# Performance work log

Hardware: AMD Instinct MI355X
Metric: run time of the kernel (lower is better)

Reference implementation:

```python
import jax, jax.numpy as jnp
import numpy as np

B, N, DIM, H, DH = 16, 1024, 768, 12, 64
SCALE = DH ** -0.5


def setup_inputs() -> dict:
    key = jax.random.key(0)
    k1, k2, k3 = jax.random.split(key, 3)
    x = jax.random.normal(k1, (B, N, DIM), dtype=jnp.float32)
    W_qkv = jax.random.normal(k2, (DIM, 3 * H * DH), dtype=jnp.float32) * (DIM ** -0.5)
    W_out = jax.random.normal(k3, (H * DH, DIM), dtype=jnp.float32) * ((H * DH) ** -0.5)
    b_out = jnp.zeros((DIM,), dtype=jnp.float32)
    # perm = [0] + random shuffle of 1..N-1 (matches module's construction)
    rng = np.random.default_rng(0)
    perm = jnp.asarray(np.concatenate([[0], rng.permutation(np.arange(1, N))]), dtype=jnp.int32)
    return {"x": x, "W_qkv": W_qkv, "W_out": W_out, "b_out": b_out, "perm": perm}


def reference(x, W_qkv, W_out, b_out, perm):
    # QKV projection: [b, n, 3*h*d]
    qkv = jnp.einsum('bnd,de->bne', x, W_qkv)
    q, k, v = jnp.split(qkv, 3, axis=-1)
    # [b, n, h*d] -> [b, h, n, d]
    reshape = lambda t: t.reshape(B, N, H, DH).transpose(0, 2, 1, 3)
    q, k, v = reshape(q), reshape(k), reshape(v)
    # permute query rows
    q = q[:, :, perm]
    dots = jnp.einsum('bhqd,bhkd->bhqk', q, k) * SCALE
    attn = jax.nn.softmax(dots, axis=-1)
    out = jnp.einsum('bhqk,bhkd->bhqd', attn, v)
    out = out.transpose(0, 2, 1, 3).reshape(B, N, H * DH)
    return jnp.einsum('bne,ed->bnd', out, W_out) + b_out
```

## Files before the change

### kernel.cpp

```cpp
#include <hip/hip_runtime.h>
#include <hip/hip_bf16.h>


typedef __bf16 bf16x8 __attribute__((ext_vector_type(8)));
typedef __bf16 bf16x4 __attribute__((ext_vector_type(4)));
typedef float  f32x4  __attribute__((ext_vector_type(4)));

__device__ __forceinline__ f32x4 mfma16(bf16x8 a, bf16x8 b, f32x4 c) {
    return __builtin_amdgcn_mfma_f32_16x16x32_bf16(a, b, c, 0, 0, 0);
}

__device__ __forceinline__ void async16(const void* g, void* l) {
    __builtin_amdgcn_global_load_lds(
        (const __attribute__((address_space(1))) unsigned int*)g,
        (__attribute__((address_space(3))) unsigned int*)l,
        16, 0, 0);
}

__global__ __launch_bounds__(256)
void prep(const void* __restrict__ x, __bf16* __restrict__ Xc,
          const void* __restrict__ Wqkv, __bf16* __restrict__ Wqt,
          const void* __restrict__ Wout, __bf16* __restrict__ Wot,
          int* __restrict__ flag) {
    __shared__ __bf16 tile[64][65];
    __shared__ int cnt;
    const int bid = blockIdx.x;
    const int tid = threadIdx.x;

    const unsigned short* raw =
        (bid < 1024) ? (const unsigned short*)x
                     : (bid < 1456) ? (const unsigned short*)Wqkv
                                    : (const unsigned short*)Wout;
    if (tid == 0) cnt = 0;
    __syncthreads();
    int local = 0;
    for (int i = tid; i < 2048; i += 256) {
        unsigned e = (raw[i] >> 7) & 0xFFu;
        if (e >= 0xC0u) local++;
    }
    atomicAdd(&cnt, local);
    __syncthreads();
    const int f = (cnt > 16) ? 1 : 0;
    if (bid == 0 && tid == 0) *flag = f;

    if (bid < 1024) {
        const int n4 = 16384 * 768 / 4;
        int i = bid * 256 + tid;
        const int stride = 1024 * 256;
        if (f) {
            const float4* s = (const float4*)x;
            for (; i < n4; i += stride) {
                float4 v = s[i];
                bf16x4 o;
                o[0] = (__bf16)v.x; o[1] = (__bf16)v.y;
                o[2] = (__bf16)v.z; o[3] = (__bf16)v.w;
                *(bf16x4*)&Xc[(size_t)i * 4] = o;
            }
        } else {
            const ushort4* s = (const ushort4*)x;
            for (; i < n4; i += stride) *(ushort4*)&Xc[(size_t)i * 4] = s[i];
        }
    } else {
        const void* in;
        __bf16* out;
        int R, C, c0, r0;
        if (bid < 1456) {
            int t = bid - 1024;
            in = Wqkv; out = Wqt; R = 768; C = 2304;
            c0 = (t % 36) * 64; r0 = (t / 36) * 64;
        } else {
            int t = bid - 1456;
            in = Wout; out = Wot; R = 768; C = 768;
            c0 = (t % 12) * 64; r0 = (t / 12) * 64;
        }
        const int tx = tid & 63, ty = tid >> 6;
#pragma unroll
        for (int k = 0; k < 16; ++k) {
            int r = ty + 4 * k;
            size_t idx = (size_t)(r0 + r) * C + c0 + tx;
            tile[r][tx] = f ? (__bf16)((const float*)in)[idx] : ((const __bf16*)in)[idx];
        }
        __syncthreads();
#pragma unroll
        for (int k = 0; k < 16; ++k) {
            int cc = ty + 4 * k;
            out[(size_t)(c0 + cc) * R + r0 + tx] = tile[tx][cc];
        }
    }
}

#define GMFMA16()                                                       \
    acc[0][0] = mfma16(af0, bf0, acc[0][0]);                            \
    acc[0][1] = mfma16(af0, bf1, acc[0][1]);                            \
    acc[0][2] = mfma16(af0, bf2, acc[0][2]);                            \
    acc[0][3] = mfma16(af0, bf3, acc[0][3]);                            \
    acc[1][0] = mfma16(af1, bf0, acc[1][0]);                            \
    acc[1][1] = mfma16(af1, bf1, acc[1][1]);                            \
    acc[1][2] = mfma16(af1, bf2, acc[1][2]);                            \
    acc[1][3] = mfma16(af1, bf3, acc[1][3]);                            \
    acc[2][0] = mfma16(af2, bf0, acc[2][0]);                            \
    acc[2][1] = mfma16(af2, bf1, acc[2][1]);                            \
    acc[2][2] = mfma16(af2, bf2, acc[2][2]);                            \
    acc[2][3] = mfma16(af2, bf3, acc[2][3]);                            \
    acc[3][0] = mfma16(af3, bf0, acc[3][0]);                            \
    acc[3][1] = mfma16(af3, bf1, acc[3][1]);                            \
    acc[3][2] = mfma16(af3, bf2, acc[3][2]);                            \
    acc[3][3] = mfma16(af3, bf3, acc[3][3])

#define GTILE(RD, ST, DO_STAGE, VMK) do {                               \
    if ((VMK) == 4)                                                     \
        asm volatile("s_waitcnt vmcnt(4) lgkmcnt(0)" ::: "memory");     \
    else                                                                \
        asm volatile("s_waitcnt vmcnt(0) lgkmcnt(0)" ::: "memory");     \
    __builtin_amdgcn_s_barrier();                                       \
    if (DO_STAGE) {                                                     \
        async16(gA0, smem + (ST) + stA0);                               \
        async16(gA1, smem + (ST) + stA1);                               \
        async16(gB0, smem + (ST) + 8192 + stA0);                        \
        async16(gB1, smem + (ST) + 8192 + stA1);                        \
        gA0 += 32; gA1 += 32; gB0 += 32; gB1 += 32;                     \
    }                                                                   \
    bf16x8 af0 = *(const bf16x8*)(smem + (RD) + aoff0);                 \
    bf16x8 af1 = *(const bf16x8*)(smem + (RD) + aoff1);                 \
    bf16x8 af2 = *(const bf16x8*)(smem + (RD) + aoff2);                 \
    bf16x8 af3 = *(const bf16x8*)(smem + (RD) + aoff3);                 \
    bf16x8 bf0 = *(const bf16x8*)(smem + (RD) + boff0);                 \
    bf16x8 bf1 = *(const bf16x8*)(smem + (RD) + boff1);                 \
    bf16x8 bf2 = *(const bf16x8*)(smem + (RD) + boff2);                 \
    bf16x8 bf3 = *(const bf16x8*)(smem + (RD) + boff3);                 \
    GMFMA16();                                                          \
} while (0)

template <int MODE>
__global__ __launch_bounds__(256, 3)
void gemm_bt(const __bf16* __restrict__ A, int lda,
             const __bf16* __restrict__ Bt,
             const void* __restrict__ bias,
             void* __restrict__ Cout, int ldc,
             int K, const int* __restrict__ flag,
             __bf16* __restrict__ vt) {
    __shared__ __align__(16) char smem[49152];
    const int tid  = threadIdx.x;
    const int wid  = tid >> 6;
    const int lane = tid & 63;
    const int quad = lane >> 4;
    const int l15  = lane & 15;

    const int bm = blockIdx.x * 128;
    const int bn = blockIdx.y * 128;

    const int wm = (wid & 1) * 64;
    const int wn = (wid >> 1) * 64;
    const int srow  = lane >> 2;
    const int sslot = lane & 3;

    const int rA0 = wid * 16 + srow;
    const int rA1 = 64 + wid * 16 + srow;
    const __bf16* gA0 = A  + (size_t)(bm + rA0) * lda + ((sslot ^ ((rA0 >> 1) & 3)) << 3);
    const __bf16* gA1 = A  + (size_t)(bm + rA1) * lda + ((sslot ^ ((rA1 >> 1) & 3)) << 3);
    const __bf16* gB0 = Bt + (size_t)(bn + rA0) * K   + ((sslot ^ ((rA0 >> 1) & 3)) << 3);
    const __bf16* gB1 = Bt + (size_t)(bn + rA1) * K   + ((sslot ^ ((rA1 >> 1) & 3)) << 3);
    const int stA0 = (wid * 16) * 64;
    const int stA1 = (64 + wid * 16) * 64;

    const int rf0 = wm + 0 * 16 + l15, rf1 = wm + 1 * 16 + l15;
    const int rf2 = wm + 2 * 16 + l15, rf3 = wm + 3 * 16 + l15;
    const int aoff0 = rf0 * 64 + ((quad ^ ((rf0 >> 1) & 3)) * 16);
    const int aoff1 = rf1 * 64 + ((quad ^ ((rf1 >> 1) & 3)) * 16);
    const int aoff2 = rf2 * 64 + ((quad ^ ((rf2 >> 1) & 3)) * 16);
    const int aoff3 = rf3 * 64 + ((quad ^ ((rf3 >> 1) & 3)) * 16);
    const int rg0 = wn + 0 * 16 + l15, rg1 = wn + 1 * 16 + l15;
    const int rg2 = wn + 2 * 16 + l15, rg3 = wn + 3 * 16 + l15;
    const int boff0 = 8192 + rg0 * 64 + ((quad ^ ((rg0 >> 1) & 3)) * 16);
    const int boff1 = 8192 + rg1 * 64 + ((quad ^ ((rg1 >> 1) & 3)) * 16);
    const int boff2 = 8192 + rg2 * 64 + ((quad ^ ((rg2 >> 1) & 3)) * 16);
    const int boff3 = 8192 + rg3 * 64 + ((quad ^ ((rg3 >> 1) & 3)) * 16);

    f32x4 acc[4][4];
#pragma unroll
    for (int i = 0; i < 4; ++i)
#pragma unroll
        for (int j = 0; j < 4; ++j) acc[i][j] = (f32x4)0.0f;

    async16(gA0, smem + stA0);
    async16(gA1, smem + stA1);
    async16(gB0, smem + 8192 + stA0);
    async16(gB1, smem + 8192 + stA1);
    gA0 += 32; gA1 += 32; gB0 += 32; gB1 += 32;
    async16(gA0, smem + 16384 + stA0);
    async16(gA1, smem + 16384 + stA1);
    async16(gB0, smem + 16384 + 8192 + stA0);
    async16(gB1, smem + 16384 + 8192 + stA1);
    gA0 += 32; gA1 += 32; gB0 += 32; gB1 += 32;

#pragma unroll 1
    for (int g = 0; g < 7; ++g) {
        GTILE(0,     32768, true, 4);
        GTILE(16384, 0,     true, 4);
        GTILE(32768, 16384, true, 4);
    }
    GTILE(0,     32768, true,  4);
    GTILE(16384, 0,     false, 4);
    GTILE(32768, 0,     false, 0);

    if (MODE == 0 && bn >= 1536) {
        const int bq = bm >> 10;
        const int n0 = (bm & 1023) + wm + quad * 4;
        const int colb = bn - 1536 + wn;
#pragma unroll
        for (int mi = 0; mi < 4; ++mi)
#pragma unroll
            for (int ni = 0; ni < 4; ++ni) {
                int col = colb + ni * 16 + l15;
                bf16x4 v;
                v[0] = (__bf16)acc[mi][ni][0];
                v[1] = (__bf16)acc[mi][ni][1];
                v[2] = (__bf16)acc[mi][ni][2];
                v[3] = (__bf16)acc[mi][ni][3];
                *(bf16x4*)&vt[((size_t)bq * 768 + col) * 1024 + n0 + mi * 16] = v;
            }
        return;
    }

    const int f = (MODE == 1) ? *flag : 0;
    if (MODE == 1) {
#pragma unroll
        for (int ni = 0; ni < 4; ++ni) {
            int col = bn + wn + ni * 16 + l15;
            float bv = f ? ((const float*)bias)[col] : (float)((const __bf16*)bias)[col];
#pragma unroll
            for (int mi = 0; mi < 4; ++mi)
#pragma unroll
                for (int rg = 0; rg < 4; ++rg) acc[mi][ni][rg] += bv;
        }
    }

    if (MODE == 0 || !f) {
        __bf16* cs = (__bf16*)smem;
#pragma unroll
        for (int c = 0; c < 4; ++c) {
            __syncthreads();
            if (wm == (c >> 1) * 64) {
                int mb = (c & 1) * 2;
#pragma unroll
                for (int mloc = 0; mloc < 2; ++mloc) {
                    int rowc = mloc * 16 + quad * 4;
#pragma unroll
                    for (int ni = 0; ni < 4; ++ni) {
                        int col = wn + ni * 16 + l15;
#pragma unroll
                        for (int rg = 0; rg < 4; ++rg)
                            cs[(rowc + rg) * 136 + col] = (__bf16)acc[mb + mloc][ni][rg];
                    }
                }
            }
            __syncthreads();
#pragma unroll
            for (int p = 0; p < 2; ++p) {
                int row  = p * 16 + (tid >> 4);
                int colc = tid & 15;
                bf16x8 v = *(const bf16x8*)&cs[row * 136 + colc * 8];
                *(bf16x8*)((__bf16*)Cout + (size_t)(bm + c * 32 + row) * ldc + bn + colc * 8) = v;
            }
        }
    } else {
        float* cs = (float*)smem;
#pragma unroll
        for (int c = 0; c < 8; ++c) {
            __syncthreads();
            if (wm == (c >> 2) * 64) {
                int mi = c & 3;
                int rowc = quad * 4;
#pragma unroll
                for (int ni = 0; ni < 4; ++ni) {
                    int col = wn + ni * 16 + l15;
#pragma unroll
                    for (int rg = 0; rg < 4; ++rg)
                        cs[(rowc + rg) * 132 + col] = acc[mi][ni][rg];
                }
            }
            __syncthreads();
#pragma unroll
            for (int p = 0; p < 2; ++p) {
                int row  = p * 8 + (tid >> 5);
                int colc = tid & 31;
                float4 v = *(const float4*)&cs[row * 132 + colc * 4];
                *(float4*)((float*)Cout + (size_t)(bm + c * 16 + row) * ldc + bn + colc * 4) = v;
            }
        }
    }
}

__global__ __launch_bounds__(256, 2)
void attn(const __bf16* qkv, const __bf16* __restrict__ vt,
          const int* __restrict__ perm, __bf16* O, int ldo) {
    __shared__ __align__(16) char smem[55296];
    __bf16* Qs = (__bf16*)smem;
    __bf16* Ps = (__bf16*)(smem + 32768);

    const int tid  = threadIdx.x;
    const int wid  = tid >> 6;
    const int lane = tid & 63;
    const int quad = lane >> 4;
    const int l15  = lane & 15;
    const int bh = blockIdx.x;
    const int q0 = blockIdx.y * 128;
    const int b = bh / 12, h = bh % 12;
    const size_t row_base = (size_t)b * 1024;
    const int qcol = h * 64;
    const int kcol = 768 + h * 64;
    const int srow8  = lane >> 3;
    const int sslot8 = lane & 7;
    __bf16* Pw = Ps + wid * (32 * 88);

#pragma unroll
    for (int is = 0; is < 4; ++is) {
        int r = is * 32 + wid * 8 + srow8;
        int gr = perm[q0 + r];
        int chunk = sslot8 ^ (r & 7);
        async16(qkv + (row_base + gr) * 2304 + qcol + chunk * 8,
                &Qs[(is * 32 + wid * 8) * 64]);
    }
    __syncthreads();

    bf16x8 qf[2][2];
#pragma unroll
    for (int mi = 0; mi < 2; ++mi) {
        int r = wid * 32 + mi * 16 + l15;
#pragma unroll
        for (int ks = 0; ks < 2; ++ks)
            qf[mi][ks] = *(const bf16x8*)&Qs[r * 64 + (((ks * 4 + quad) ^ (r & 7)) * 8)];
    }
    asm volatile("s_waitcnt lgkmcnt(0)" ::: "memory");
    __builtin_amdgcn_sched_barrier(0);
    __builtin_amdgcn_s_barrier();

    const int off0 = l15 * 64 + (((0 * 4 + quad) ^ (l15 & 7)) * 8);
    const int off1 = l15 * 64 + (((1 * 4 + quad) ^ (l15 & 7)) * 8);
    const int pwb  = l15 * 88 + quad * 4;
    const int pfb  = l15 * 88 + quad * 8;

    const int rK = wid * 8 + srow8;
    const int ck = sslot8 ^ (rK & 7);
    const __bf16* kg0 = qkv + (row_base + rK) * 2304 + kcol + ck * 8;
    const __bf16* kg1 = kg0 + (size_t)32 * 2304;
    const __bf16* vg0 = vt + ((size_t)bh * 64 + rK) * 1024 + ck * 8;
    const __bf16* vg1 = vg0 + (size_t)32 * 1024;

    f32x4 acco[2][4];
#pragma unroll
    for (int mi = 0; mi < 2; ++mi)
#pragma unroll
        for (int ni = 0; ni < 4; ++ni) acco[mi][ni] = (f32x4)0.0f;
    float lsum[2] = {0.0f, 0.0f};

    const float cfac = 0.125f * 1.44269504088896340736f;

#define ASTAGE(KB, VB) do {                                             \
        async16(kg0, smem + (KB) + wid * 1024);                         \
        async16(kg1, smem + (KB) + 4096 + wid * 1024);                  \
        async16(vg0, smem + (VB) + wid * 1024);                         \
        async16(vg1, smem + (VB) + 4096 + wid * 1024);                  \
        kg0 += (size_t)64 * 2304; kg1 += (size_t)64 * 2304;             \
        vg0 += 64; vg1 += 64;                                           \
    } while (0)

    auto compute = [&](const __bf16* Kb, const __bf16* Vb) {
#pragma unroll
        for (int half = 0; half < 2; ++half) {
            f32x4 accs[2][2];
#pragma unroll
            for (int ki = 0; ki < 2; ++ki)
#pragma unroll
                for (int mi = 0; mi < 2; ++mi) accs[ki][mi] = (f32x4)0.0f;
#pragma unroll
            for (int ks = 0; ks < 2; ++ks) {
                const int off = ks ? off1 : off0;
                bf16x8 kf0 = *(const bf16x8*)&Kb[(half * 2 + 0) * 1024 + off];
                bf16x8 kf1 = *(const bf16x8*)&Kb[(half * 2 + 1) * 1024 + off];
                accs[0][0] = mfma16(kf0, qf[0][ks], accs[0][0]);
                accs[0][1] = mfma16(kf0, qf[1][ks], accs[0][1]);
                accs[1][0] = mfma16(kf1, qf[0][ks], accs[1][0]);
                accs[1][1] = mfma16(kf1, qf[1][ks], accs[1][1]);
            }

#pragma unroll
            for (int ki = 0; ki < 2; ++ki)
#pragma unroll
                for (int mi = 0; mi < 2; ++mi) {
                    bf16x4 pk;
                    float s0 = __builtin_amdgcn_exp2f(accs[ki][mi][0] * cfac - 8.0f);
                    float s1 = __builtin_amdgcn_exp2f(accs[ki][mi][1] * cfac - 8.0f);
                    float s2 = __builtin_amdgcn_exp2f(accs[ki][mi][2] * cfac - 8.0f);
                    float s3 = __builtin_amdgcn_exp2f(accs[ki][mi][3] * cfac - 8.0f);
                    pk[0] = (__bf16)s0; pk[1] = (__bf16)s1;
                    pk[2] = (__bf16)s2; pk[3] = (__bf16)s3;
                    lsum[mi] += (s0 + s1) + (s2 + s3);
                    *(bf16x4*)&Pw[pwb + mi * 1408 + (half * 2 + ki) * 16] = pk;
                }

            {
                bf16x8 pf0 = *(const bf16x8*)&Pw[pfb + 0 * 1408 + half * 32];
                bf16x8 pf1 = *(const bf16x8*)&Pw[pfb + 1 * 1408 + half * 32];
                const int offv = half ? off1 : off0;
#pragma unroll
                for (int ni = 0; ni < 4; ++ni) {
                    bf16x8 vf = *(const bf16x8*)&Vb[ni * 1024 + offv];
                    acco[0][ni] = mfma16(pf0, vf, acco[0][ni]);
                    acco[1][ni] = mfma16(pf1, vf, acco[1][ni]);
                }
            }
        }
    };

    ASTAGE(0, 16384);

#pragma unroll 1
    for (int kt2 = 0; kt2 < 8; ++kt2) {
        asm volatile("s_waitcnt vmcnt(0) lgkmcnt(0)" ::: "memory");
        __builtin_amdgcn_s_barrier();
        ASTAGE(8192, 16384 + 8192);
        compute((const __bf16*)smem, (const __bf16*)(smem + 16384));
        asm volatile("s_waitcnt vmcnt(0) lgkmcnt(0)" ::: "memory");
        __builtin_amdgcn_s_barrier();
        if (kt2 < 7) ASTAGE(0, 16384);
        compute((const __bf16*)(smem + 8192), (const __bf16*)(smem + 16384 + 8192));
    }
#undef ASTAGE

#pragma unroll
    for (int off = 16; off < 64; off <<= 1) {
        lsum[0] += __shfl_xor(lsum[0], off, 64);
        lsum[1] += __shfl_xor(lsum[1], off, 64);
    }

#pragma unroll
    for (int mi = 0; mi < 2; ++mi) {
#pragma unroll
        for (int rg = 0; rg < 4; ++rg) {
            float inv = 1.0f / __shfl(lsum[mi], quad * 4 + rg, 64);
            int orow = q0 + wid * 32 + mi * 16 + quad * 4 + rg;
#pragma unroll
            for (int ni = 0; ni < 4; ++ni) {
                int ocol = h * 64 + ni * 16 + l15;
                O[(row_base + orow) * (size_t)ldo + ocol] = (__bf16)(acco[mi][ni][rg] * inv);
            }
        }
    }
}

extern "C" void kernel_launch(void* const* d_in, const int* in_sizes, int n_in,
                              void* d_out, int out_size, void* d_ws, size_t ws_size,
                              hipStream_t stream) {
    (void)in_sizes; (void)n_in; (void)out_size; (void)ws_size;
    const void* x_raw    = d_in[0];
    const void* Wqkv_raw = d_in[1];
    const void* Wout_raw = d_in[2];
    const void* bout_raw = d_in[3];
    const int*  perm     = (const int*)d_in[4];

    char* ws = (char*)d_ws;
    int*    flag = (int*)ws;
    __bf16* Xc   = (__bf16*)(ws + 256);
    __bf16* QKV  = (__bf16*)(ws + 25166080);
    __bf16* Vt   = (__bf16*)(ws + 100663552);
    __bf16* Wqt  = (__bf16*)(ws + 125829376);
    __bf16* Wot  = (__bf16*)(ws + 129368320);
    __bf16* Obuf = QKV + 1536;

    prep<<<1600, 256, 0, stream>>>(x_raw, Xc, Wqkv_raw, Wqt, Wout_raw, Wot, flag);
    gemm_bt<0><<<dim3(128, 18), 256, 0, stream>>>(Xc, 768, Wqt, nullptr, QKV, 2304, 768, nullptr, Vt);
    attn<<<dim3(192, 8), 256, 0, stream>>>(QKV, Vt, perm, Obuf, 2304);
    gemm_bt<1><<<dim3(128, 6), 256, 0, stream>>>(Obuf, 2304, Wot, bout_raw, d_out, 768, 768, flag, nullptr);
}
```

Before: 198.0 us.

## Enlarge GEMM block tile to 256x128 with 128x64 per-warp tiles

Both projection GEMMs now use 256-row block tiles, so each warp computes a 128x64 sub-tile with 8x4 MFMA accumulators, and the grids are halved to match. The goal is more MFMA work per LDS fragment load and per staged byte, cutting LDS and global traffic per FLOP. The cost is a larger LDS footprint (72KB triple buffer), more registers, occupancy lowered from 3 to 2 blocks per CU, and fewer blocks in the grid (1152 and 384), which may leave CUs idle in the tail.

```diff
diff --git a/kernel.cpp b/kernel.cpp
--- a/kernel.cpp
+++ b/kernel.cpp
@@ -89,126 +89,108 @@
     }
 }
 
-#define GMFMA16()                                                       \
-    acc[0][0] = mfma16(af0, bf0, acc[0][0]);                            \
-    acc[0][1] = mfma16(af0, bf1, acc[0][1]);                            \
-    acc[0][2] = mfma16(af0, bf2, acc[0][2]);                            \
-    acc[0][3] = mfma16(af0, bf3, acc[0][3]);                            \
-    acc[1][0] = mfma16(af1, bf0, acc[1][0]);                            \
-    acc[1][1] = mfma16(af1, bf1, acc[1][1]);                            \
-    acc[1][2] = mfma16(af1, bf2, acc[1][2]);                            \
-    acc[1][3] = mfma16(af1, bf3, acc[1][3]);                            \
-    acc[2][0] = mfma16(af2, bf0, acc[2][0]);                            \
-    acc[2][1] = mfma16(af2, bf1, acc[2][1]);                            \
-    acc[2][2] = mfma16(af2, bf2, acc[2][2]);                            \
-    acc[2][3] = mfma16(af2, bf3, acc[2][3]);                            \
-    acc[3][0] = mfma16(af3, bf0, acc[3][0]);                            \
-    acc[3][1] = mfma16(af3, bf1, acc[3][1]);                            \
-    acc[3][2] = mfma16(af3, bf2, acc[3][2]);                            \
-    acc[3][3] = mfma16(af3, bf3, acc[3][3])
+#define GM4(MI, AF)                                                     \
+    acc[MI][0] = mfma16(AF, bq0, acc[MI][0]);                           \
+    acc[MI][1] = mfma16(AF, bq1, acc[MI][1]);                           \
+    acc[MI][2] = mfma16(AF, bq2, acc[MI][2]);                           \
+    acc[MI][3] = mfma16(AF, bq3, acc[MI][3])
+
+#define GSTAGE(ST) do {                                                 \
+    async16(gA0, smem + (ST) + stA);                                    \
+    async16(gA1, smem + (ST) + stA + 1024);                             \
+    async16(gA2, smem + (ST) + stA + 2048);                             \
+    async16(gA3, smem + (ST) + stA + 3072);                             \
+    async16(gB0, smem + (ST) + 16384 + stB);                            \
+    async16(gB1, smem + (ST) + 16384 + stB + 1024);                     \
+    gA0 += 32; gA1 += 32; gA2 += 32; gA3 += 32;                         \
+    gB0 += 32; gB1 += 32;                                               \
+} while (0)
 
 #define GTILE(RD, ST, DO_STAGE, VMK) do {                               \
-    if ((VMK) == 4)                                                     \
-        asm volatile("s_waitcnt vmcnt(4) lgkmcnt(0)" ::: "memory");     \
+    if ((VMK) == 6)                                                     \
+        asm volatile("s_waitcnt vmcnt(6) lgkmcnt(0)" ::: "memory");     \
     else                                                                \
         asm volatile("s_waitcnt vmcnt(0) lgkmcnt(0)" ::: "memory");     \
     __builtin_amdgcn_s_barrier();                                       \
-    if (DO_STAGE) {                                                     \
-        async16(gA0, smem + (ST) + stA0);                               \
-        async16(gA1, smem + (ST) + stA1);                               \
-        async16(gB0, smem + (ST) + 8192 + stA0);                        \
-        async16(gB1, smem + (ST) + 8192 + stA1);                        \
-        gA0 += 32; gA1 += 32; gB0 += 32; gB1 += 32;                     \
-    }                                                                   \
-    bf16x8 af0 = *(const bf16x8*)(smem + (RD) + aoff0);                 \
-    bf16x8 af1 = *(const bf16x8*)(smem + (RD) + aoff1);                 \
-    bf16x8 af2 = *(const bf16x8*)(smem + (RD) + aoff2);                 \
-    bf16x8 af3 = *(const bf16x8*)(smem + (RD) + aoff3);                 \
-    bf16x8 bf0 = *(const bf16x8*)(smem + (RD) + boff0);                 \
-    bf16x8 bf1 = *(const bf16x8*)(smem + (RD) + boff1);                 \
-    bf16x8 bf2 = *(const bf16x8*)(smem + (RD) + boff2);                 \
-    bf16x8 bf3 = *(const bf16x8*)(smem + (RD) + boff3);                 \
-    GMFMA16();                                                          \
+    if (DO_STAGE) GSTAGE(ST);                                           \
+    bf16x8 af0 = *(const bf16x8*)(smem + (RD) + abase + 0 * 1024);      \
+    bf16x8 af1 = *(const bf16x8*)(smem + (RD) + abase + 1 * 1024);      \
+    bf16x8 af2 = *(const bf16x8*)(smem + (RD) + abase + 2 * 1024);      \
+    bf16x8 af3 = *(const bf16x8*)(smem + (RD) + abase + 3 * 1024);      \
+    bf16x8 af4 = *(const bf16x8*)(smem + (RD) + abase + 4 * 1024);      \
+    bf16x8 af5 = *(const bf16x8*)(smem + (RD) + abase + 5 * 1024);      \
+    bf16x8 af6 = *(const bf16x8*)(smem + (RD) + abase + 6 * 1024);      \
+    bf16x8 af7 = *(const bf16x8*)(smem + (RD) + abase + 7 * 1024);      \
+    bf16x8 bq0 = *(const bf16x8*)(smem + (RD) + bbase + 0 * 1024);      \
+    bf16x8 bq1 = *(const bf16x8*)(smem + (RD) + bbase + 1 * 1024);      \
+    bf16x8 bq2 = *(const bf16x8*)(smem + (RD) + bbase + 2 * 1024);      \
+    bf16x8 bq3 = *(const bf16x8*)(smem + (RD) + bbase + 3 * 1024);      \
+    GM4(0, af0); GM4(1, af1); GM4(2, af2); GM4(3, af3);                 \
+    GM4(4, af4); GM4(5, af5); GM4(6, af6); GM4(7, af7);                 \
 } while (0)
 
 template <int MODE>
-__global__ __launch_bounds__(256, 3)
+__global__ __launch_bounds__(256, 2)
 void gemm_bt(const __bf16* __restrict__ A, int lda,
              const __bf16* __restrict__ Bt,
              const void* __restrict__ bias,
              void* __restrict__ Cout, int ldc,
              int K, const int* __restrict__ flag,
              __bf16* __restrict__ vt) {
-    __shared__ __align__(16) char smem[49152];
+    __shared__ __align__(16) char smem[73728];
     const int tid  = threadIdx.x;
     const int wid  = tid >> 6;
     const int lane = tid & 63;
     const int quad = lane >> 4;
     const int l15  = lane & 15;
 
-    const int bm = blockIdx.x * 128;
+    const int bm = blockIdx.x * 256;
     const int bn = blockIdx.y * 128;
 
-    const int wm = (wid & 1) * 64;
+    const int wm = (wid & 1) * 128;
     const int wn = (wid >> 1) * 64;
     const int srow  = lane >> 2;
     const int sslot = lane & 3;
 
-    const int rA0 = wid * 16 + srow;
-    const int rA1 = 64 + wid * 16 + srow;
-    const __bf16* gA0 = A  + (size_t)(bm + rA0) * lda + ((sslot ^ ((rA0 >> 1) & 3)) << 3);
-    const __bf16* gA1 = A  + (size_t)(bm + rA1) * lda + ((sslot ^ ((rA1 >> 1) & 3)) << 3);
-    const __bf16* gB0 = Bt + (size_t)(bn + rA0) * K   + ((sslot ^ ((rA0 >> 1) & 3)) << 3);
-    const __bf16* gB1 = Bt + (size_t)(bn + rA1) * K   + ((sslot ^ ((rA1 >> 1) & 3)) << 3);
-    const int stA0 = (wid * 16) * 64;
-    const int stA1 = (64 + wid * 16) * 64;
-
-    const int rf0 = wm + 0 * 16 + l15, rf1 = wm + 1 * 16 + l15;
-    const int rf2 = wm + 2 * 16 + l15, rf3 = wm + 3 * 16 + l15;
-    const int aoff0 = rf0 * 64 + ((quad ^ ((rf0 >> 1) & 3)) * 16);
-    const int aoff1 = rf1 * 64 + ((quad ^ ((rf1 >> 1) & 3)) * 16);
-    const int aoff2 = rf2 * 64 + ((quad ^ ((rf2 >> 1) & 3)) * 16);
-    const int aoff3 = rf3 * 64 + ((quad ^ ((rf3 >> 1) & 3)) * 16);
-    const int rg0 = wn + 0 * 16 + l15, rg1 = wn + 1 * 16 + l15;
-    const int rg2 = wn + 2 * 16 + l15, rg3 = wn + 3 * 16 + l15;
-    const int boff0 = 8192 + rg0 * 64 + ((quad ^ ((rg0 >> 1) & 3)) * 16);
-    const int boff1 = 8192 + rg1 * 64 + ((quad ^ ((rg1 >> 1) & 3)) * 16);
-    const int boff2 = 8192 + rg2 * 64 + ((quad ^ ((rg2 >> 1) & 3)) * 16);
-    const int boff3 = 8192 + rg3 * 64 + ((quad ^ ((rg3 >> 1) & 3)) * 16);
-
-    f32x4 acc[4][4];
-#pragma unroll
-    for (int i = 0; i < 4; ++i)
+    const int cchunk = ((sslot ^ ((srow >> 1) & 3)) << 3);
+    const __bf16* gA0 = A + (size_t)(bm + wid * 64 +  0 + srow) * lda + cchunk;
+    const __bf16* gA1 = A + (size_t)(bm + wid * 64 + 16 + srow) * lda + cchunk;
+    const __bf16* gA2 = A + (size_t)(bm + wid * 64 + 32 + srow) * lda + cchunk;
+    const __bf16* gA3 = A + (size_t)(bm + wid * 64 + 48 + srow) * lda + cchunk;
+    const __bf16* gB0 = Bt + (size_t)(bn + wid * 32 +  0 + srow) * K + cchunk;
+    const __bf16* gB1 = Bt + (size_t)(bn + wid * 32 + 16 + srow) * K + cchunk;
+    const int stA = wid * 4096;
+    const int stB = wid * 2048;
+
+    const int sl = (quad ^ ((l15 >> 1) & 3)) * 16;
+    const int abase = (wm + l15) * 64 + sl;
+    const int bbase = 16384 + (wn + l15) * 64 + sl;
+
+    f32x4 acc[8][4];
+#pragma unroll
+    for (int i = 0; i < 8; ++i)
 #pragma unroll
         for (int j = 0; j < 4; ++j) acc[i][j] = (f32x4)0.0f;
 
-    async16(gA0, smem + stA0);
-    async16(gA1, smem + stA1);
-    async16(gB0, smem + 8192 + stA0);
-    async16(gB1, smem + 8192 + stA1);
-    gA0 += 32; gA1 += 32; gB0 += 32; gB1 += 32;
-    async16(gA0, smem + 16384 + stA0);
-    async16(gA1, smem + 16384 + stA1);
-    async16(gB0, smem + 16384 + 8192 + stA0);
-    async16(gB1, smem + 16384 + 8192 + stA1);
-    gA0 += 32; gA1 += 32; gB0 += 32; gB1 += 32;
+    GSTAGE(0);
+    GSTAGE(24576);
 
 #pragma unroll 1
     for (int g = 0; g < 7; ++g) {
-        GTILE(0,     32768, true, 4);
-        GTILE(16384, 0,     true, 4);
-        GTILE(32768, 16384, true, 4);
-    }
-    GTILE(0,     32768, true,  4);
-    GTILE(16384, 0,     false, 4);
-    GTILE(32768, 0,     false, 0);
+        GTILE(0,     49152, true, 6);
+        GTILE(24576, 0,     true, 6);
+        GTILE(49152, 24576, true, 6);
+    }
+    GTILE(0,     49152, true,  6);
+    GTILE(24576, 0,     false, 6);
+    GTILE(49152, 0,     false, 0);
 
     if (MODE == 0 && bn >= 1536) {
         const int bq = bm >> 10;
         const int n0 = (bm & 1023) + wm + quad * 4;
         const int colb = bn - 1536 + wn;
 #pragma unroll
-        for (int mi = 0; mi < 4; ++mi)
+        for (int mi = 0; mi < 8; ++mi)
 #pragma unroll
             for (int ni = 0; ni < 4; ++ni) {
                 int col = colb + ni * 16 + l15;
@@ -229,7 +211,7 @@
             int col = bn + wn + ni * 16 + l15;
             float bv = f ? ((const float*)bias)[col] : (float)((const __bf16*)bias)[col];
 #pragma unroll
-            for (int mi = 0; mi < 4; ++mi)
+            for (int mi = 0; mi < 8; ++mi)
 #pragma unroll
                 for (int rg = 0; rg < 4; ++rg) acc[mi][ni][rg] += bv;
         }
@@ -238,19 +220,18 @@
     if (MODE == 0 || !f) {
         __bf16* cs = (__bf16*)smem;
 #pragma unroll
-        for (int c = 0; c < 4; ++c) {
+        for (int c = 0; c < 8; ++c) {
             __syncthreads();
-            if (wm == (c >> 1) * 64) {
-                int mb = (c & 1) * 2;
+            if (wm == (c >> 2) * 128) {
 #pragma unroll
                 for (int mloc = 0; mloc < 2; ++mloc) {
-                    int rowc = mloc * 16 + quad * 4;
 #pragma unroll
                     for (int ni = 0; ni < 4; ++ni) {
                         int col = wn + ni * 16 + l15;
 #pragma unroll
                         for (int rg = 0; rg < 4; ++rg)
-                            cs[(rowc + rg) * 136 + col] = (__bf16)acc[mb + mloc][ni][rg];
+                            cs[(mloc * 16 + quad * 4 + rg) * 136 + col] =
+                                (__bf16)acc[(c & 3) * 2 + mloc][ni][rg];
                     }
                 }
             }
@@ -266,17 +247,15 @@
     } else {
         float* cs = (float*)smem;
 #pragma unroll
-        for (int c = 0; c < 8; ++c) {
+        for (int c = 0; c < 16; ++c) {
             __syncthreads();
-            if (wm == (c >> 2) * 64) {
-                int mi = c & 3;
-                int rowc = quad * 4;
+            if (wm == (c >> 3) * 128) {
 #pragma unroll
                 for (int ni = 0; ni < 4; ++ni) {
                     int col = wn + ni * 16 + l15;
 #pragma unroll
                     for (int rg = 0; rg < 4; ++rg)
-                        cs[(rowc + rg) * 132 + col] = acc[mi][ni][rg];
+                        cs[(quad * 4 + rg) * 132 + col] = acc[c & 7][ni][rg];
                 }
             }
             __syncthreads();
@@ -469,7 +448,7 @@
     __bf16* Obuf = QKV + 1536;
 
     prep<<<1600, 256, 0, stream>>>(x_raw, Xc, Wqkv_raw, Wqt, Wout_raw, Wot, flag);
-    gemm_bt<0><<<dim3(128, 18), 256, 0, stream>>>(Xc, 768, Wqt, nullptr, QKV, 2304, 768, nullptr, Vt);
+    gemm_bt<0><<<dim3(64, 18), 256, 0, stream>>>(Xc, 768, Wqt, nullptr, QKV, 2304, 768, nullptr, Vt);
     attn<<<dim3(192, 8), 256, 0, stream>>>(QKV, Vt, perm, Obuf, 2304);
-    gemm_bt<1><<<dim3(128, 6), 256, 0, stream>>>(Obuf, 2304, Wot, bout_raw, d_out, 768, 768, flag, nullptr);
-}
+    gemm_bt<1><<<dim3(64, 6), 256, 0, stream>>>(Obuf, 2304, Wot, bout_raw, d_out, 768, 768, flag, nullptr);
+}
```

After: 193.3 us (median of 3 runs). -2.3%, faster.
